# Kernel tuning notes

Hardware: AMD Instinct MI355X
Metric: run time of the kernel (lower is better)

## Reference

```python
import jax, jax.numpy as jnp
import numpy as np

B, NB, K, C, CM, POS = 8, 1024, 9, 32, 128, 2
SIGMA = 0.5
NEG_SLOPE = 0.01  # nn.LeakyReLU default
BN_EPS = 1e-5


def _leaky(x):
    return jnp.where(x >= 0, x, NEG_SLOPE * x)


def _batchnorm(x, gamma, beta):
    # BatchNorm1d, training-mode batch statistics over the point dimension
    mu = jnp.mean(x, axis=0)
    var = jnp.mean((x - mu) ** 2, axis=0)
    return gamma * (x - mu) * jax.lax.rsqrt(var + BN_EPS) + beta


def setup_inputs() -> dict:
    key = jax.random.key(0)
    ks = jax.random.split(key, 8)
    N = B * NB
    positions = jax.random.normal(ks[0], (N, POS), jnp.float32)
    weights = jax.random.normal(ks[1], (N, C), jnp.float32)
    batch = jnp.full((B,), NB, dtype=jnp.int32)  # uniform point counts per graph
    # KernelConv params: kernel_init='grid' -> 3x3 grid of offsets spanning +-sigma
    g = jnp.linspace(-SIGMA, SIGMA, 3, dtype=jnp.float32)
    kernel_positions = jnp.stack(jnp.meshgrid(g, g, indexing='ij'), axis=-1).reshape(K, POS)
    kernel_weights = (jax.random.normal(ks[2], (K, C, C), jnp.float32) / np.float32(np.sqrt(C * K)))
    conv_norm_gamma = jnp.ones((C,), jnp.float32)
    conv_norm_beta = jnp.zeros((C,), jnp.float32)
    # PyG MLP([C, CM, C+POS], act_first=True, plain_last=True)
    W1 = jax.random.normal(ks[3], (C, CM), jnp.float32) / np.float32(np.sqrt(C))
    b1 = jnp.zeros((CM,), jnp.float32)
    bn_gamma = jnp.ones((CM,), jnp.float32)
    bn_beta = jnp.zeros((CM,), jnp.float32)
    W2 = jax.random.normal(ks[4], (CM, C + POS), jnp.float32) / np.float32(np.sqrt(CM))
    b2 = jnp.zeros((C + POS,), jnp.float32)
    return dict(positions=positions, weights=weights, batch=batch,
                kernel_positions=kernel_positions, kernel_weights=kernel_weights,
                conv_norm_gamma=conv_norm_gamma, conv_norm_beta=conv_norm_beta,
                W1=W1, b1=b1, bn_gamma=bn_gamma, bn_beta=bn_beta, W2=W2, b2=b2)


def reference(positions, weights, batch, kernel_positions, kernel_weights,
              conv_norm_gamma, conv_norm_beta, W1, b1, bn_gamma, bn_beta, W2, b2):
    N = positions.shape[0]
    # --- KernelConv: each point spawns K components at pos + kernel offset ---
    conv_pos = (positions[:, None, :] + kernel_positions[None, :, :])  # [N,K,2]
    conv_w = jnp.einsum('nc,kcd->nkd', weights, kernel_weights)        # [N,K,C]
    conv_pos = conv_pos.reshape(B, NB * K, POS)
    conv_w = conv_w.reshape(B, NB * K, C)
    # --- KernelSample: evaluate Gaussian mixture at original positions ---
    p = positions.reshape(B, NB, POS)
    d2 = (jnp.sum(p * p, -1)[:, :, None]
          + jnp.sum(conv_pos * conv_pos, -1)[:, None, :]
          - 2.0 * jnp.einsum('bnd,bmd->bnm', p, conv_pos))             # [B,NB,NB*K]
    Kmat = jnp.exp(-d2 / (2.0 * SIGMA * SIGMA))
    sampled = jnp.einsum('bnm,bmc->bnc', Kmat, conv_w).reshape(N, C)
    x = _leaky(sampled)                                                 # KernelSample nonlinearity
    # conv_norm + residual add of input weights
    x = _batchnorm(x, conv_norm_gamma, conv_norm_beta) + weights
    # MLP: lin -> act -> batchnorm (act_first) -> plain last lin
    h = _batchnorm(_leaky(x @ W1 + b1), bn_gamma, bn_beta)
    mlp_out = h @ W2 + b2                                               # [N, POS + C]
    delta_pos, delta_w = mlp_out[:, :POS], mlp_out[:, POS:]
    return positions + delta_pos, x + delta_w
```

## Files before the change

kernel.cpp:

```cpp
#include <hip/hip_runtime.h>
#include <hip/hip_bf16.h>

#define BB    8
#define NBB   1024
#define KK    9
#define CC    32
#define CMM   128
#define NTOT  (BB*NBB)
#define MM    (NBB*KK)
#define NEG   0.01f
#define EPS   1e-5f
#define SQL2  1.6986436f

#define OFF_CWT   0
#define SZ_CWT    (BB*CC*MM/2)
#define OFF_QPX   (OFF_CWT + SZ_CWT)
#define OFF_QPY   (OFF_QPX + BB*MM)
#define OFF_X0    (OFF_QPY + BB*MM)
#define OFF_X     (OFF_X0 + NTOT*CC)
#define OFF_H0    (OFF_X + NTOT*CC)
#define OFF_ST    (OFF_H0 + NTOT*CMM)

typedef __attribute__((ext_vector_type(8))) short short8;
typedef __attribute__((ext_vector_type(4))) float f32x4;
typedef __attribute__((ext_vector_type(2))) float f32x2;

static __device__ __forceinline__ unsigned short f2bf_rne(float f) {
    __hip_bfloat16 h = __float2bfloat16(f);
    return *reinterpret_cast<unsigned short*>(&h);
}


__global__ __launch_bounds__(256) void k_convw(const float* __restrict__ pos,
                                               const float* __restrict__ kpos,
                                               const float* __restrict__ w,
                                               const float* __restrict__ kw,
                                               float* __restrict__ qpx,
                                               float* __restrict__ qpy,
                                               float* __restrict__ stats,
                                               short* __restrict__ cwT) {
    __shared__ unsigned short kwl[KK*CC*CC];
    __shared__ unsigned short tile[9*32*32];
    int t = threadIdx.x;
    int l = t & 63, wv = t >> 6;
    int lane15 = l & 15, quad = l >> 4;
    int blk = blockIdx.x;
    int b = blk & 7, nbl = blk >> 3;

    if (blk == 0 && t < 320) stats[t] = 0.f;
    #pragma unroll
    for (int rep = 0; rep < 2; ++rep) {
        int gid = rep*65536 + blk*256 + t;
        if (gid < BB*MM) {
            int bb = gid / MM;
            int m = gid - bb*MM;
            int np = m / 9, k9 = m - np*9;
            float qx = pos[((size_t)(bb*NBB + np))*2 + 0] + kpos[k9*2 + 0];
            float qy = pos[((size_t)(bb*NBB + np))*2 + 1] + kpos[k9*2 + 1];
            qpx[gid] = SQL2*qx;
            qpy[gid] = SQL2*qy;
        }
    }
    for (int u = t; u < KK*CC*CC/4; u += 256) {
        int flat = u*4;
        int row = flat >> 5;
        int c0 = flat & 31;
        int kk = row >> 5, cp = row & 31;
        f32x4 v = *(const f32x4*)&kw[flat];
        kwl[(kk*CC + c0+0)*CC + cp] = f2bf_rne(v.x);
        kwl[(kk*CC + c0+1)*CC + cp] = f2bf_rne(v.y);
        kwl[(kk*CC + c0+2)*CC + cp] = f2bf_rne(v.z);
        kwl[(kk*CC + c0+3)*CC + cp] = f2bf_rne(v.w);
    }
    int n = b*NBB + nbl*32 + (wv & 1)*16 + lane15;
    f32x4 w0 = *(const f32x4*)&w[(size_t)n*CC + quad*8];
    f32x4 w1 = *(const f32x4*)&w[(size_t)n*CC + quad*8 + 4];
    union { unsigned short us[8]; short8 s; } bfr;
    bfr.us[0] = f2bf_rne(w0.x); bfr.us[1] = f2bf_rne(w0.y);
    bfr.us[2] = f2bf_rne(w0.z); bfr.us[3] = f2bf_rne(w0.w);
    bfr.us[4] = f2bf_rne(w1.x); bfr.us[5] = f2bf_rne(w1.y);
    bfr.us[6] = f2bf_rne(w1.z); bfr.us[7] = f2bf_rne(w1.w);
    __syncthreads();
    if (wv < 2) {
        f32x4 acc[KK][2];
        #pragma unroll
        for (int kk = 0; kk < KK; ++kk)
            #pragma unroll
            for (int ct = 0; ct < 2; ++ct) {
                int c = ct*16 + lane15;
                short8 afr = *(const short8*)&kwl[(kk*CC + c)*CC + quad*8];
                acc[kk][ct] = __builtin_amdgcn_mfma_f32_16x16x32_bf16(
                    afr, bfr.s, (f32x4)0.f, 0, 0, 0);
            }
        #pragma unroll
        for (int kk = 0; kk < KK; ++kk) {
            int ml = (wv*16 + lane15)*9 + kk;
            unsigned short* tw = &tile[(ml >> 5)*1024 + (ml & 31)];
            #pragma unroll
            for (int ct = 0; ct < 2; ++ct)
                #pragma unroll
                for (int reg = 0; reg < 4; ++reg) {
                    int c = ct*16 + quad*4 + reg;
                    tw[c*32] = f2bf_rne(acc[kk][ct][reg]);
                }
        }
    }
    __syncthreads();
    short* dst = cwT + (size_t)b*CC*MM + (size_t)nbl*9216;
    #pragma unroll
    for (int it = 0; it < 5; ++it) {
        int u = it*256 + t;
        if (u < 1152) {
            short8 v = *(const short8*)&tile[u*8];
            *(short8*)&dst[u*8] = v;
        }
    }
}

__global__ __launch_bounds__(1024, 4) void k_sample(const float* __restrict__ pos,
                                                    const float* __restrict__ qpx,
                                                    const float* __restrict__ qpy,
                                                    const short* __restrict__ cwT,
                                                    float* __restrict__ x0,
                                                    float* __restrict__ s1) {
    __shared__ float red[16*32*36];
    __shared__ float sstat[64];
    int t = threadIdx.x;
    int l = t & 63, wv = t >> 6;
    int blk = blockIdx.x;
    int b = blk & 7, nblk = blk >> 3;
    int lane15 = l & 15, quad = l >> 4;
    int nbase = b*NBB + nblk*32;
    if (t < 64) sstat[t] = 0.f;

    float px[2], py[2];
    #pragma unroll
    for (int nt = 0; nt < 2; ++nt) {
        int n = nbase + nt*16 + lane15;
        px[nt] = SQL2*pos[(size_t)n*2];
        py[nt] = SQL2*pos[(size_t)n*2 + 1];
    }
    f32x4 acc[2][2];
    acc[0][0] = (f32x4)0.f; acc[0][1] = (f32x4)0.f;
    acc[1][0] = (f32x4)0.f; acc[1][1] = (f32x4)0.f;

    const float* qx = qpx + (size_t)b*MM;
    const float* qy = qpy + (size_t)b*MM;
    const short* cab = cwT + (size_t)b*CC*MM + (size_t)lane15*32 + quad*8;

    int m0 = wv*576 + quad*8;
    int ma = (wv*18) * 1024;
    short8 a0 = *(const short8*)&cab[ma];
    short8 a1 = *(const short8*)&cab[ma + 512];
    f32x4 X0 = *(const f32x4*)&qx[m0], X1 = *(const f32x4*)&qx[m0 + 4];
    f32x4 Y0 = *(const f32x4*)&qy[m0], Y1 = *(const f32x4*)&qy[m0 + 4];
    for (int kk = 0; kk < 18; ++kk) {
        int step = (kk < 17) ? 1 : 0;
        int mn = m0 + step*32;
        int man = ma + step*1024;
        short8 na0 = *(const short8*)&cab[man];
        short8 na1 = *(const short8*)&cab[man + 512];
        f32x4 nX0 = *(const f32x4*)&qx[mn], nX1 = *(const f32x4*)&qx[mn + 4];
        f32x4 nY0 = *(const f32x4*)&qy[mn], nY1 = *(const f32x4*)&qy[mn + 4];
        #pragma unroll
        for (int nt = 0; nt < 2; ++nt) {
            f32x2 PX = {px[nt], px[nt]};
            f32x2 PY = {py[nt], py[nt]};
            f32x2 dx0 = (f32x2){X0.x, X0.y} - PX;
            f32x2 dy0 = (f32x2){Y0.x, Y0.y} - PY;
            f32x2 t0 = dx0*dx0; t0 = dy0*dy0 + t0;
            f32x2 dx1 = (f32x2){X0.z, X0.w} - PX;
            f32x2 dy1 = (f32x2){Y0.z, Y0.w} - PY;
            f32x2 t1 = dx1*dx1; t1 = dy1*dy1 + t1;
            f32x2 dx2 = (f32x2){X1.x, X1.y} - PX;
            f32x2 dy2 = (f32x2){Y1.x, Y1.y} - PY;
            f32x2 t2 = dx2*dx2; t2 = dy2*dy2 + t2;
            f32x2 dx3 = (f32x2){X1.z, X1.w} - PX;
            f32x2 dy3 = (f32x2){Y1.z, Y1.w} - PY;
            f32x2 t3 = dx3*dx3; t3 = dy3*dy3 + t3;
            float e0 = __builtin_amdgcn_exp2f(-t0.x);
            float e1 = __builtin_amdgcn_exp2f(-t0.y);
            float e2 = __builtin_amdgcn_exp2f(-t1.x);
            float e3 = __builtin_amdgcn_exp2f(-t1.y);
            float e4 = __builtin_amdgcn_exp2f(-t2.x);
            float e5 = __builtin_amdgcn_exp2f(-t2.y);
            float e6 = __builtin_amdgcn_exp2f(-t3.x);
            float e7 = __builtin_amdgcn_exp2f(-t3.y);
            union { unsigned int u[4]; short8 s; } bf;
            bf.u[0] = (__float_as_uint(e0) >> 16) | (__float_as_uint(e1) & 0xffff0000u);
            bf.u[1] = (__float_as_uint(e2) >> 16) | (__float_as_uint(e3) & 0xffff0000u);
            bf.u[2] = (__float_as_uint(e4) >> 16) | (__float_as_uint(e5) & 0xffff0000u);
            bf.u[3] = (__float_as_uint(e6) >> 16) | (__float_as_uint(e7) & 0xffff0000u);
            acc[nt][0] = __builtin_amdgcn_mfma_f32_16x16x32_bf16(a0, bf.s, acc[nt][0], 0, 0, 0);
            acc[nt][1] = __builtin_amdgcn_mfma_f32_16x16x32_bf16(a1, bf.s, acc[nt][1], 0, 0, 0);
        }
        a0 = na0; a1 = na1;
        X0 = nX0; X1 = nX1; Y0 = nY0; Y1 = nY1;
        m0 = mn; ma = man;
    }
    #pragma unroll
    for (int nt = 0; nt < 2; ++nt)
        #pragma unroll
        for (int ct = 0; ct < 2; ++ct) {
            int nn = nt*16 + lane15, c = ct*16 + quad*4;
            *(f32x4*)&red[(wv*32 + nn)*36 + c] = acc[nt][ct];
        }
    __syncthreads();
    if (t < 256) {
        int nr = t >> 3, c0 = (t & 7)*4;
        f32x4 v = (f32x4)0.f;
        #pragma unroll
        for (int wp = 0; wp < 16; ++wp)
            v = v + *(const f32x4*)&red[(wp*32 + nr)*36 + c0];
        v.x = v.x >= 0.f ? v.x : NEG*v.x;
        v.y = v.y >= 0.f ? v.y : NEG*v.y;
        v.z = v.z >= 0.f ? v.z : NEG*v.z;
        v.w = v.w >= 0.f ? v.w : NEG*v.w;
        *(f32x4*)&x0[((size_t)(nbase + nr))*CC + c0] = v;
        float s0 = v.x, s1v = v.y, s2v = v.z, s3v = v.w;
        float q0 = v.x*v.x, q1 = v.y*v.y, q2 = v.z*v.z, q3 = v.w*v.w;
        #pragma unroll
        for (int mk = 8; mk <= 32; mk <<= 1) {
            s0 += __shfl_xor(s0, mk); s1v += __shfl_xor(s1v, mk);
            s2v += __shfl_xor(s2v, mk); s3v += __shfl_xor(s3v, mk);
            q0 += __shfl_xor(q0, mk); q1 += __shfl_xor(q1, mk);
            q2 += __shfl_xor(q2, mk); q3 += __shfl_xor(q3, mk);
        }
        if (l < 8) {
            atomicAdd(&sstat[c0 + 0], s0);  atomicAdd(&sstat[c0 + 1], s1v);
            atomicAdd(&sstat[c0 + 2], s2v); atomicAdd(&sstat[c0 + 3], s3v);
            atomicAdd(&sstat[32 + c0 + 0], q0); atomicAdd(&sstat[32 + c0 + 1], q1);
            atomicAdd(&sstat[32 + c0 + 2], q2); atomicAdd(&sstat[32 + c0 + 3], q3);
        }
    }
    __syncthreads();
    if (t < 64) atomicAdd(&s1[t], sstat[t]);
}

__global__ __launch_bounds__(256) void k_mlp1(const float* __restrict__ x0,
                                              const float* __restrict__ wts,
                                              const float* __restrict__ gma,
                                              const float* __restrict__ bta,
                                              const float* __restrict__ W1,
                                              const float* __restrict__ b1,
                                              const float* __restrict__ s1,
                                              float* __restrict__ x,
                                              float* __restrict__ h0,
                                              float* __restrict__ s2) {
    __shared__ float tile[32*68];
    int t = threadIdx.x;
    int l = t & 63, wv = t >> 6;
    int blk = blockIdx.x;
    int nb = blk >> 2, jq = blk & 3;
    int n = nb*64 + l;
    int j0 = jq*32 + wv*8;

    float xv[32];
    #pragma unroll
    for (int c = 0; c < 32; ++c) {
        float mu  = s1[c] * (1.f/NTOT);
        float var = s1[32+c]*(1.f/NTOT) - mu*mu;
        float a   = gma[c] * rsqrtf(var + EPS);
        float v   = x0[(size_t)n*CC + c];
        xv[c] = a*(v - mu) + bta[c] + wts[(size_t)n*CC + c];
    }
    if (jq == 0 && wv == 0) {
        #pragma unroll
        for (int c = 0; c < 32; c += 4)
            *(float4*)&x[(size_t)n*CC + c] = make_float4(xv[c], xv[c+1], xv[c+2], xv[c+3]);
    }
    float acc[8];
    *(f32x4*)&acc[0] = *(const f32x4*)&b1[j0];
    *(f32x4*)&acc[4] = *(const f32x4*)&b1[j0 + 4];
    #pragma unroll 8
    for (int c = 0; c < 32; ++c) {
        float xc = xv[c];
        const float* w1r = W1 + c*CMM + j0;
        f32x4 wa = *(const f32x4*)&w1r[0];
        f32x4 wb = *(const f32x4*)&w1r[4];
        acc[0] = fmaf(xc, wa.x, acc[0]); acc[1] = fmaf(xc, wa.y, acc[1]);
        acc[2] = fmaf(xc, wa.z, acc[2]); acc[3] = fmaf(xc, wa.w, acc[3]);
        acc[4] = fmaf(xc, wb.x, acc[4]); acc[5] = fmaf(xc, wb.y, acc[5]);
        acc[6] = fmaf(xc, wb.z, acc[6]); acc[7] = fmaf(xc, wb.w, acc[7]);
    }
    #pragma unroll
    for (int jj = 0; jj < 8; ++jj) {
        acc[jj] = acc[jj] >= 0.f ? acc[jj] : NEG*acc[jj];
        tile[(wv*8 + jj)*68 + l] = acc[jj];
    }
    float* hd = h0 + (size_t)n*CMM + j0;
    *(float4*)&hd[0] = make_float4(acc[0], acc[1], acc[2], acc[3]);
    *(float4*)&hd[4] = make_float4(acc[4], acc[5], acc[6], acc[7]);
    __syncthreads();
    if (t < 256) {
        int jl = t >> 3, grp = t & 7;
        float lsum = 0.f, lsq = 0.f;
        #pragma unroll
        for (int q = 0; q < 2; ++q) {
            f32x4 v = *(const f32x4*)&tile[jl*68 + grp*8 + q*4];
            lsum += v.x + v.y + v.z + v.w;
            lsq = fmaf(v.x, v.x, fmaf(v.y, v.y, fmaf(v.z, v.z, fmaf(v.w, v.w, lsq))));
        }
        lsum += __shfl_xor(lsum, 1); lsq += __shfl_xor(lsq, 1);
        lsum += __shfl_xor(lsum, 2); lsq += __shfl_xor(lsq, 2);
        lsum += __shfl_xor(lsum, 4); lsq += __shfl_xor(lsq, 4);
        if (grp == 0) {
            int jg = jq*32 + jl;
            atomicAdd(&s2[jg], lsum);
            atomicAdd(&s2[CMM + jg], lsq);
        }
    }
}

__global__ __launch_bounds__(256) void k_mlp2(const float* __restrict__ h0,
                                              const float* __restrict__ x,
                                              const float* __restrict__ pos,
                                              const float* __restrict__ g2,
                                              const float* __restrict__ bt2,
                                              const float* __restrict__ W2,
                                              const float* __restrict__ b2,
                                              const float* __restrict__ s2,
                                              float* __restrict__ out) {
    __shared__ float red[16*16*35];
    int t = threadIdx.x;
    int nl = t & 15, rid = t >> 4;
    int n = blockIdx.x*16 + nl;
    int j0 = rid*8;
    float hv[8];
    *(f32x4*)&hv[0] = *(const f32x4*)&h0[(size_t)n*CMM + j0];
    *(f32x4*)&hv[4] = *(const f32x4*)&h0[(size_t)n*CMM + j0 + 4];
    #pragma unroll
    for (int jj = 0; jj < 8; ++jj) {
        int j = j0 + jj;
        float mu  = s2[j] * (1.f/NTOT);
        float var = s2[CMM+j]*(1.f/NTOT) - mu*mu;
        float a   = g2[j] * rsqrtf(var + EPS);
        hv[jj] = a*(hv[jj] - mu) + bt2[j];
    }
    float acc[34];
    #pragma unroll
    for (int c = 0; c < 34; ++c) acc[c] = 0.f;
    for (int jj = 0; jj < 8; ++jj) {
        float h = hv[jj];
        const float* w2r = W2 + (size_t)(j0 + jj)*34;
        #pragma unroll
        for (int c = 0; c < 34; ++c)
            acc[c] = fmaf(h, w2r[c], acc[c]);
    }
    #pragma unroll
    for (int c = 0; c < 34; ++c) red[(rid*16 + nl)*35 + c] = acc[c];
    __syncthreads();
    #pragma unroll
    for (int it = 0; it < 3; ++it) {
        int u = it*256 + t;
        if (u < 544) {
            int r = u / 34, c = u - r*34;
            float v = b2[c];
            #pragma unroll
            for (int rr = 0; rr < 16; ++rr) v += red[(rr*16 + r)*35 + c];
            int nn = blockIdx.x*16 + r;
            if (c < 2)
                out[(size_t)nn*2 + c] = pos[(size_t)nn*2 + c] + v;
            else
                out[16384 + (size_t)nn*32 + (c-2)] = x[(size_t)nn*32 + (c-2)] + v;
        }
    }
}

extern "C" void kernel_launch(void* const* d_in, const int* in_sizes, int n_in,
                              void* d_out, int out_size, void* d_ws, size_t ws_size,
                              hipStream_t stream) {
    const float* positions = (const float*)d_in[0];
    const float* weights   = (const float*)d_in[1];
    const float* kpos = (const float*)d_in[3];
    const float* kw   = (const float*)d_in[4];
    const float* cg   = (const float*)d_in[5];
    const float* cb   = (const float*)d_in[6];
    const float* W1   = (const float*)d_in[7];
    const float* b1   = (const float*)d_in[8];
    const float* bg   = (const float*)d_in[9];
    const float* bb   = (const float*)d_in[10];
    const float* W2   = (const float*)d_in[11];
    const float* b2   = (const float*)d_in[12];
    float* ws  = (float*)d_ws;
    float* out = (float*)d_out;

    float* s1 = ws + OFF_ST;
    float* s2 = ws + OFF_ST + 64;

    k_convw<<<256, 256, 0, stream>>>(positions, kpos, weights, kw,
                                     ws + OFF_QPX, ws + OFF_QPY,
                                     s1, (short*)(ws + OFF_CWT));
    k_sample<<<256, 1024, 0, stream>>>(positions, ws + OFF_QPX, ws + OFF_QPY,
                                       (const short*)(ws + OFF_CWT),
                                       ws + OFF_X0, s1);
    k_mlp1<<<512, 256, 0, stream>>>(ws + OFF_X0, weights, cg, cb, W1, b1,
                                    s1, ws + OFF_X, ws + OFF_H0, s2);
    k_mlp2<<<512, 256, 0, stream>>>(ws + OFF_H0, ws + OFF_X, positions,
                                    bg, bb, W2, b2, s2, out);
}
```

Baseline: 143.6 us.

## Triple-buffer sample loop loads, spread conv-weight MFMA over all waves, use perm packing

The Gaussian-sample loop now keeps three register sets of operand loads in flight, each fetched two iterations ahead instead of one, to hide global-memory latency behind the exp and MFMA work. Packing bf16 pairs now uses a single v_perm per pair instead of shift, mask and or. In the conv-weight precompute kernel, four waves each compute one 16-row channel half instead of two waves computing both halves, spreading the MFMA work over more waves. The cost is higher register pressure in a kernel launched at 1024 threads with occupancy bound 4, which may cause spills. There are also redundant clamped loads at the loop tail.

```diff
diff --git a/kernel.cpp b/kernel.cpp
--- a/kernel.cpp
+++ b/kernel.cpp
@@ -81,28 +81,25 @@
     bfr.us[4] = f2bf_rne(w1.x); bfr.us[5] = f2bf_rne(w1.y);
     bfr.us[6] = f2bf_rne(w1.z); bfr.us[7] = f2bf_rne(w1.w);
     __syncthreads();
-    if (wv < 2) {
-        f32x4 acc[KK][2];
-        #pragma unroll
-        for (int kk = 0; kk < KK; ++kk)
-            #pragma unroll
-            for (int ct = 0; ct < 2; ++ct) {
-                int c = ct*16 + lane15;
-                short8 afr = *(const short8*)&kwl[(kk*CC + c)*CC + quad*8];
-                acc[kk][ct] = __builtin_amdgcn_mfma_f32_16x16x32_bf16(
-                    afr, bfr.s, (f32x4)0.f, 0, 0, 0);
-            }
+    {
+        int ntile = wv & 1, cth = wv >> 1;
+        f32x4 acc[KK];
         #pragma unroll
         for (int kk = 0; kk < KK; ++kk) {
-            int ml = (wv*16 + lane15)*9 + kk;
+            int c = cth*16 + lane15;
+            short8 afr = *(const short8*)&kwl[(kk*CC + c)*CC + quad*8];
+            acc[kk] = __builtin_amdgcn_mfma_f32_16x16x32_bf16(
+                afr, bfr.s, (f32x4)0.f, 0, 0, 0);
+        }
+        #pragma unroll
+        for (int kk = 0; kk < KK; ++kk) {
+            int ml = (ntile*16 + lane15)*9 + kk;
             unsigned short* tw = &tile[(ml >> 5)*1024 + (ml & 31)];
             #pragma unroll
-            for (int ct = 0; ct < 2; ++ct)
-                #pragma unroll
-                for (int reg = 0; reg < 4; ++reg) {
-                    int c = ct*16 + quad*4 + reg;
-                    tw[c*32] = f2bf_rne(acc[kk][ct][reg]);
-                }
+            for (int reg = 0; reg < 4; ++reg) {
+                int c = cth*16 + quad*4 + reg;
+                tw[c*32] = f2bf_rne(acc[kk][reg]);
+            }
         }
     }
     __syncthreads();
@@ -116,6 +113,51 @@
         }
     }
 }
+
+#define LOADSET(A0,A1,XX0,XX1,YY0,YY1,it) do { \
+    int _i = (it) < 18 ? (it) : 17; \
+    int _m = wvm + _i*32; \
+    int _a = _i*1024; \
+    A0 = *(const short8*)&cab[_a]; \
+    A1 = *(const short8*)&cab[_a + 512]; \
+    XX0 = *(const f32x4*)&qx[_m]; XX1 = *(const f32x4*)&qx[_m + 4]; \
+    YY0 = *(const f32x4*)&qy[_m]; YY1 = *(const f32x4*)&qy[_m + 4]; \
+} while (0)
+
+#define COMPUTE(A0,A1,XX0,XX1,YY0,YY1) do { \
+    _Pragma("unroll") \
+    for (int nt = 0; nt < 2; ++nt) { \
+        f32x2 PX = {px[nt], px[nt]}; \
+        f32x2 PY = {py[nt], py[nt]}; \
+        f32x2 dx0 = (f32x2){XX0.x, XX0.y} - PX; \
+        f32x2 dy0 = (f32x2){YY0.x, YY0.y} - PY; \
+        f32x2 t0 = dx0*dx0; t0 = dy0*dy0 + t0; \
+        f32x2 dx1 = (f32x2){XX0.z, XX0.w} - PX; \
+        f32x2 dy1 = (f32x2){YY0.z, YY0.w} - PY; \
+        f32x2 t1 = dx1*dx1; t1 = dy1*dy1 + t1; \
+        f32x2 dx2 = (f32x2){XX1.x, XX1.y} - PX; \
+        f32x2 dy2 = (f32x2){YY1.x, YY1.y} - PY; \
+        f32x2 t2 = dx2*dx2; t2 = dy2*dy2 + t2; \
+        f32x2 dx3 = (f32x2){XX1.z, XX1.w} - PX; \
+        f32x2 dy3 = (f32x2){YY1.z, YY1.w} - PY; \
+        f32x2 t3 = dx3*dx3; t3 = dy3*dy3 + t3; \
+        float e0 = __builtin_amdgcn_exp2f(-t0.x); \
+        float e1 = __builtin_amdgcn_exp2f(-t0.y); \
+        float e2 = __builtin_amdgcn_exp2f(-t1.x); \
+        float e3 = __builtin_amdgcn_exp2f(-t1.y); \
+        float e4 = __builtin_amdgcn_exp2f(-t2.x); \
+        float e5 = __builtin_amdgcn_exp2f(-t2.y); \
+        float e6 = __builtin_amdgcn_exp2f(-t3.x); \
+        float e7 = __builtin_amdgcn_exp2f(-t3.y); \
+        union { unsigned int u[4]; short8 s; } bf; \
+        bf.u[0] = __builtin_amdgcn_perm(__float_as_uint(e1), __float_as_uint(e0), 0x07060302u); \
+        bf.u[1] = __builtin_amdgcn_perm(__float_as_uint(e3), __float_as_uint(e2), 0x07060302u); \
+        bf.u[2] = __builtin_amdgcn_perm(__float_as_uint(e5), __float_as_uint(e4), 0x07060302u); \
+        bf.u[3] = __builtin_amdgcn_perm(__float_as_uint(e7), __float_as_uint(e6), 0x07060302u); \
+        acc[nt][0] = __builtin_amdgcn_mfma_f32_16x16x32_bf16(A0, bf.s, acc[nt][0], 0, 0, 0); \
+        acc[nt][1] = __builtin_amdgcn_mfma_f32_16x16x32_bf16(A1, bf.s, acc[nt][1], 0, 0, 0); \
+    } \
+} while (0)
 
 __global__ __launch_bounds__(1024, 4) void k_sample(const float* __restrict__ pos,
                                                     const float* __restrict__ qpx,
@@ -146,57 +188,23 @@
 
     const float* qx = qpx + (size_t)b*MM;
     const float* qy = qpy + (size_t)b*MM;
-    const short* cab = cwT + (size_t)b*CC*MM + (size_t)lane15*32 + quad*8;
-
-    int m0 = wv*576 + quad*8;
-    int ma = (wv*18) * 1024;
-    short8 a0 = *(const short8*)&cab[ma];
-    short8 a1 = *(const short8*)&cab[ma + 512];
-    f32x4 X0 = *(const f32x4*)&qx[m0], X1 = *(const f32x4*)&qx[m0 + 4];
-    f32x4 Y0 = *(const f32x4*)&qy[m0], Y1 = *(const f32x4*)&qy[m0 + 4];
-    for (int kk = 0; kk < 18; ++kk) {
-        int step = (kk < 17) ? 1 : 0;
-        int mn = m0 + step*32;
-        int man = ma + step*1024;
-        short8 na0 = *(const short8*)&cab[man];
-        short8 na1 = *(const short8*)&cab[man + 512];
-        f32x4 nX0 = *(const f32x4*)&qx[mn], nX1 = *(const f32x4*)&qx[mn + 4];
-        f32x4 nY0 = *(const f32x4*)&qy[mn], nY1 = *(const f32x4*)&qy[mn + 4];
-        #pragma unroll
-        for (int nt = 0; nt < 2; ++nt) {
-            f32x2 PX = {px[nt], px[nt]};
-            f32x2 PY = {py[nt], py[nt]};
-            f32x2 dx0 = (f32x2){X0.x, X0.y} - PX;
-            f32x2 dy0 = (f32x2){Y0.x, Y0.y} - PY;
-            f32x2 t0 = dx0*dx0; t0 = dy0*dy0 + t0;
-            f32x2 dx1 = (f32x2){X0.z, X0.w} - PX;
-            f32x2 dy1 = (f32x2){Y0.z, Y0.w} - PY;
-            f32x2 t1 = dx1*dx1; t1 = dy1*dy1 + t1;
-            f32x2 dx2 = (f32x2){X1.x, X1.y} - PX;
-            f32x2 dy2 = (f32x2){Y1.x, Y1.y} - PY;
-            f32x2 t2 = dx2*dx2; t2 = dy2*dy2 + t2;
-            f32x2 dx3 = (f32x2){X1.z, X1.w} - PX;
-            f32x2 dy3 = (f32x2){Y1.z, Y1.w} - PY;
-            f32x2 t3 = dx3*dx3; t3 = dy3*dy3 + t3;
-            float e0 = __builtin_amdgcn_exp2f(-t0.x);
-            float e1 = __builtin_amdgcn_exp2f(-t0.y);
-            float e2 = __builtin_amdgcn_exp2f(-t1.x);
-            float e3 = __builtin_amdgcn_exp2f(-t1.y);
-            float e4 = __builtin_amdgcn_exp2f(-t2.x);
-            float e5 = __builtin_amdgcn_exp2f(-t2.y);
-            float e6 = __builtin_amdgcn_exp2f(-t3.x);
-            float e7 = __builtin_amdgcn_exp2f(-t3.y);
-            union { unsigned int u[4]; short8 s; } bf;
-            bf.u[0] = (__float_as_uint(e0) >> 16) | (__float_as_uint(e1) & 0xffff0000u);
-            bf.u[1] = (__float_as_uint(e2) >> 16) | (__float_as_uint(e3) & 0xffff0000u);
-            bf.u[2] = (__float_as_uint(e4) >> 16) | (__float_as_uint(e5) & 0xffff0000u);
-            bf.u[3] = (__float_as_uint(e6) >> 16) | (__float_as_uint(e7) & 0xffff0000u);
-            acc[nt][0] = __builtin_amdgcn_mfma_f32_16x16x32_bf16(a0, bf.s, acc[nt][0], 0, 0, 0);
-            acc[nt][1] = __builtin_amdgcn_mfma_f32_16x16x32_bf16(a1, bf.s, acc[nt][1], 0, 0, 0);
-        }
-        a0 = na0; a1 = na1;
-        X0 = nX0; X1 = nX1; Y0 = nY0; Y1 = nY1;
-        m0 = mn; ma = man;
+    const short* cab = cwT + (size_t)b*CC*MM + (size_t)(wv*18)*1024
+                     + (size_t)lane15*32 + quad*8;
+    const int wvm = wv*576 + quad*8;
+
+    short8 a0A, a1A, a0B, a1B, a0C, a1C;
+    f32x4 X0A, X1A, Y0A, Y1A, X0B, X1B, Y0B, Y1B, X0C, X1C, Y0C, Y1C;
+    LOADSET(a0A, a1A, X0A, X1A, Y0A, Y1A, 0);
+    LOADSET(a0B, a1B, X0B, X1B, Y0B, Y1B, 1);
+    LOADSET(a0C, a1C, X0C, X1C, Y0C, Y1C, 2);
+    for (int i = 0; i < 6; ++i) {
+        int base = i*3;
+        COMPUTE(a0A, a1A, X0A, X1A, Y0A, Y1A);
+        LOADSET(a0A, a1A, X0A, X1A, Y0A, Y1A, base + 3);
+        COMPUTE(a0B, a1B, X0B, X1B, Y0B, Y1B);
+        LOADSET(a0B, a1B, X0B, X1B, Y0B, Y1B, base + 4);
+        COMPUTE(a0C, a1C, X0C, X1C, Y0C, Y1C);
+        LOADSET(a0C, a1C, X0C, X1C, Y0C, Y1C, base + 5);
     }
     #pragma unroll
     for (int nt = 0; nt < 2; ++nt)
```

After: 145.0 us. About the same (+1.0%).
